# Optimization experiments

Measured on AMD Instinct MI355X. Metric: run time of the kernel, lower is better.

## Reference

```python
import jax, jax.numpy as jnp
import numpy as np

B = 8
D_MODEL = 512
N_HEADS = 8
D_HEAD = 64
D_FF = 2048
N_ENC = 4
N_DEC = 4
SRC_LEN = 512
TGT_LEN = 512
PRED_LEN = 96
SRC_SIZE = 16
TGT_SIZE = 8
EPS = 1e-5
W_SCALE = 0.02


def setup_inputs() -> dict:
    key = jax.random.key(0)
    ks = iter(jax.random.split(key, 64))

    def w(shape):
        return jax.random.normal(next(ks), shape, dtype=jnp.float32) * W_SCALE

    d, f = D_MODEL, D_FF
    inp = {
        "src": jax.random.normal(next(ks), (B, SRC_LEN, SRC_SIZE), dtype=jnp.float32),
        "tgt": jax.random.normal(next(ks), (B, TGT_LEN, TGT_SIZE), dtype=jnp.float32),
        "src_pos_emb": w((SRC_LEN, d)),
        "tgt_pos_emb": w((TGT_LEN, d)),
        "src_lin_w": w((SRC_SIZE, d)), "src_lin_b": jnp.zeros((d,), jnp.float32),
        "tgt_lin_w": w((TGT_SIZE, d)), "tgt_lin_b": jnp.zeros((d,), jnp.float32),
        # encoder stacks [N_ENC, ...]
        "enc_wq": w((N_ENC, d, d)), "enc_wk": w((N_ENC, d, d)),
        "enc_wv": w((N_ENC, d, d)), "enc_wo": w((N_ENC, d, d)),
        "enc_ff1_w": w((N_ENC, d, f)), "enc_ff1_b": jnp.zeros((N_ENC, f), jnp.float32),
        "enc_ff2_w": w((N_ENC, f, d)), "enc_ff2_b": jnp.zeros((N_ENC, d), jnp.float32),
        "enc_ln1_g": jnp.ones((N_ENC, d), jnp.float32), "enc_ln1_b": jnp.zeros((N_ENC, d), jnp.float32),
        "enc_ln2_g": jnp.ones((N_ENC, d), jnp.float32), "enc_ln2_b": jnp.zeros((N_ENC, d), jnp.float32),
        # decoder stacks [N_DEC, ...]
        "dec_sa_wq": w((N_DEC, d, d)), "dec_sa_wk": w((N_DEC, d, d)),
        "dec_sa_wv": w((N_DEC, d, d)), "dec_sa_wo": w((N_DEC, d, d)),
        "dec_ca_wq": w((N_DEC, d, d)), "dec_ca_wk": w((N_DEC, d, d)),
        "dec_ca_wv": w((N_DEC, d, d)), "dec_ca_wo": w((N_DEC, d, d)),
        "dec_ff1_w": w((N_DEC, d, f)), "dec_ff1_b": jnp.zeros((N_DEC, f), jnp.float32),
        "dec_ff2_w": w((N_DEC, f, d)), "dec_ff2_b": jnp.zeros((N_DEC, d), jnp.float32),
        "dec_ln1_g": jnp.ones((N_DEC, d), jnp.float32), "dec_ln1_b": jnp.zeros((N_DEC, d), jnp.float32),
        "dec_ln2_g": jnp.ones((N_DEC, d), jnp.float32), "dec_ln2_b": jnp.zeros((N_DEC, d), jnp.float32),
        "dec_ln3_g": jnp.ones((N_DEC, d), jnp.float32), "dec_ln3_b": jnp.zeros((N_DEC, d), jnp.float32),
        "proj_w": w((d, TGT_SIZE)), "proj_b": jnp.zeros((TGT_SIZE,), jnp.float32),
    }
    return inp


def layer_norm(x, g, b):
    mu = jnp.mean(x, axis=-1, keepdims=True)
    var = jnp.mean(jnp.square(x - mu), axis=-1, keepdims=True)
    return (x - mu) * jax.lax.rsqrt(var + EPS) * g + b


def mha(x_q, x_kv, wq, wk, wv, wo, mask):
    Bq, Lq, _ = x_q.shape
    Lk = x_kv.shape[1]
    q = (x_q @ wq).reshape(Bq, Lq, N_HEADS, D_HEAD)
    k = (x_kv @ wk).reshape(Bq, Lk, N_HEADS, D_HEAD)
    v = (x_kv @ wv).reshape(Bq, Lk, N_HEADS, D_HEAD)
    scores = jnp.einsum("bqhd,bkhd->bhqk", q, k) / jnp.sqrt(
        jnp.asarray(D_HEAD, jnp.float32))
    if mask is not None:
        scores = scores + mask  # broadcast over batch/heads
    attn = jax.nn.softmax(scores, axis=-1)
    ctx = jnp.einsum("bhqk,bkhd->bqhd", attn, v).reshape(Bq, Lq, N_HEADS * D_HEAD)
    return ctx @ wo


def dec_self_mask():
    # get_subsequence_mask with pt=0: -inf on last PRED_LEN key columns
    m = jnp.zeros((TGT_LEN, TGT_LEN), jnp.float32)
    return m.at[:, -PRED_LEN:].set(-jnp.inf)


def reference(src, tgt, src_pos_emb, tgt_pos_emb, src_lin_w, src_lin_b,
              tgt_lin_w, tgt_lin_b,
              enc_wq, enc_wk, enc_wv, enc_wo, enc_ff1_w, enc_ff1_b,
              enc_ff2_w, enc_ff2_b, enc_ln1_g, enc_ln1_b, enc_ln2_g, enc_ln2_b,
              dec_sa_wq, dec_sa_wk, dec_sa_wv, dec_sa_wo,
              dec_ca_wq, dec_ca_wk, dec_ca_wv, dec_ca_wo,
              dec_ff1_w, dec_ff1_b, dec_ff2_w, dec_ff2_b,
              dec_ln1_g, dec_ln1_b, dec_ln2_g, dec_ln2_b, dec_ln3_g, dec_ln3_b,
              proj_w, proj_b):
    # input projections + positional embedding (dropout disabled, eval mode)
    enc_x = src_pos_emb[None] + src @ src_lin_w + src_lin_b
    dec_x = tgt_pos_emb[None] + tgt @ tgt_lin_w + tgt_lin_b

    # encoder (enc_self_attn_mask is None)
    for i in range(N_ENC):
        a = mha(enc_x, enc_x, enc_wq[i], enc_wk[i], enc_wv[i], enc_wo[i], None)
        enc_x = layer_norm(a + enc_x, enc_ln1_g[i], enc_ln1_b[i])
        h = jax.nn.relu(enc_x @ enc_ff1_w[i] + enc_ff1_b[i]) @ enc_ff2_w[i] + enc_ff2_b[i]
        enc_x = layer_norm(h + enc_x, enc_ln2_g[i], enc_ln2_b[i])

    sa_mask = dec_self_mask()  # [tgt_len, tgt_len]
    for i in range(N_DEC):
        a = mha(dec_x, dec_x, dec_sa_wq[i], dec_sa_wk[i], dec_sa_wv[i],
                dec_sa_wo[i], sa_mask)
        dec_x = layer_norm(a + dec_x, dec_ln1_g[i], dec_ln1_b[i])
        a = mha(dec_x, enc_x, dec_ca_wq[i], dec_ca_wk[i], dec_ca_wv[i],
                dec_ca_wo[i], None)
        dec_x = layer_norm(a + dec_x, dec_ln2_g[i], dec_ln2_b[i])
        h = jax.nn.relu(dec_x @ dec_ff1_w[i] + dec_ff1_b[i]) @ dec_ff2_w[i] + dec_ff2_b[i]
        dec_x = layer_norm(h + dec_x, dec_ln3_g[i], dec_ln3_b[i])

    return dec_x @ proj_w + proj_b  # [B, tgt_len, tgt_size]
```

## Files before the change

### kernel.cpp

```cpp
#include <hip/hip_runtime.h>
#include <hip/hip_bf16.h>
#include <math.h>

#define D_MODEL 512
#define N_HEADS 8
#define D_HEAD  64
#define D_FF    2048
#define SEQ     512
#define BATCH   8
#define ROWS    (BATCH * SEQ)
#define PRED_LEN 96
#define KLEN_MASKED (SEQ - PRED_LEN)
#define LN_EPS  1e-5f

typedef float  f32x4 __attribute__((ext_vector_type(4)));
typedef short  s16x8 __attribute__((ext_vector_type(8)));

__device__ __forceinline__ float bf2f(ushort u) {
    union { unsigned int i; float f; } c; c.i = ((unsigned int)u) << 16; return c.f;
}
__device__ __forceinline__ ushort f2bf(float v) {
    __hip_bfloat16 h = __float2bfloat16(v);
    return *(ushort*)&h;
}
__device__ __forceinline__ void gl_lds16(const void* g, void* lds) {
    __builtin_amdgcn_global_load_lds(
        (const __attribute__((address_space(1))) unsigned int*)g,
        (__attribute__((address_space(3))) unsigned int*)lds, 16, 0, 0);
}

struct GDesc {
    const ushort* A; int lda;
    const ushort* Bt; int ldb;
    ushort* C; int ldc;
    int N; int K;
    const float* bias; int relu;
    ushort* VT; int vcol0;
};

__device__ __forceinline__ void gemm_body(const GDesc& d)
{
    __shared__ __attribute__((aligned(16))) ushort As[2][128 * 64];
    __shared__ __attribute__((aligned(16))) ushort Bs[2][64 * 64];
    const int tid = threadIdx.x;
    const int w = tid >> 6, lane = tid & 63;
    const int l16 = lane & 15, quad = lane >> 4;
    const int m0 = blockIdx.y * 128, n0 = blockIdx.x * 64;
    const ushort* Ab = d.A + (size_t)m0 * d.lda;
    const ushort* Bb = d.Bt + (size_t)n0 * d.ldb;
    const int wm = (w >> 1) * 64, wn = (w & 1) * 32;
    const int nk = d.K >> 6;
    const int lr = lane >> 3, lc = lane & 7;
    const int ch = lc ^ lr;

    auto stage = [&](int buf, int k0) {
        #pragma unroll
        for (int q = 0; q < 4; ++q) {
            int seg = q * 4 + w;
            int row = seg * 8 + lr;
            gl_lds16(Ab + (size_t)row * d.lda + k0 + ch * 8,
                     (void*)(As[buf] + seg * 512));
        }
        #pragma unroll
        for (int q = 0; q < 2; ++q) {
            int seg = q * 4 + w;
            int row = seg * 8 + lr;
            gl_lds16(Bb + (size_t)row * d.ldb + k0 + ch * 8,
                     (void*)(Bs[buf] + seg * 512));
        }
    };

    f32x4 acc[4][2];
    #pragma unroll
    for (int i = 0; i < 4; ++i)
        #pragma unroll
        for (int j = 0; j < 2; ++j) acc[i][j] = (f32x4)0.f;

    auto compute = [&](int buf) {
        #pragma unroll
        for (int t2 = 0; t2 < 2; ++t2) {
            s16x8 af[4];
            #pragma unroll
            for (int i = 0; i < 4; ++i) {
                int r = wm + i * 16 + l16;
                int p = (t2 * 4 + quad) ^ (r & 7);
                af[i] = *(const s16x8*)(As[buf] + r * 64 + p * 8);
            }
            #pragma unroll
            for (int j = 0; j < 2; ++j) {
                int r = wn + j * 16 + l16;
                int p = (t2 * 4 + quad) ^ (r & 7);
                s16x8 bfr = *(const s16x8*)(Bs[buf] + r * 64 + p * 8);
                #pragma unroll
                for (int i = 0; i < 4; ++i)
                    acc[i][j] = __builtin_amdgcn_mfma_f32_16x16x32_bf16(af[i], bfr, acc[i][j], 0, 0, 0);
            }
        }
    };

    stage(0, 0);
    __syncthreads();
    int cur = 0;
    for (int t = 0; t < nk - 1; ++t) {
        stage(cur ^ 1, (t + 1) << 6);
        compute(cur);
        __syncthreads();
        cur ^= 1;
    }
    compute(cur);

    const bool isv = (d.VT != nullptr) && (n0 >= d.vcol0);
    if (isv) {
        #pragma unroll
        for (int i = 0; i < 4; ++i) {
            int mrow = m0 + wm + i * 16 + quad * 4;
            int b = mrow >> 9, pbase = mrow & 511;
            #pragma unroll
            for (int j = 0; j < 2; ++j) {
                int cv = n0 + wn + j * 16 + l16 - d.vcol0;
                int h = cv >> 6, dd = cv & 63;
                union { ushort u[4]; uint2 v; } pk;
                #pragma unroll
                for (int r = 0; r < 4; ++r) pk.u[r] = f2bf(acc[i][j][r]);
                *(uint2*)(d.VT + ((size_t)((b * 8 + h) * 64 + dd) * 512 + pbase)) = pk.v;
            }
        }
    } else {
        #pragma unroll
        for (int i = 0; i < 4; ++i) {
            #pragma unroll
            for (int j = 0; j < 2; ++j) {
                int col = n0 + wn + j * 16 + l16;
                float bv = d.bias ? d.bias[col] : 0.f;
                #pragma unroll
                for (int r = 0; r < 4; ++r) {
                    float v = acc[i][j][r] + bv;
                    if (d.relu) v = fmaxf(v, 0.f);
                    d.C[(size_t)(m0 + wm + i * 16 + quad * 4 + r) * d.ldc + col] = f2bf(v);
                }
            }
        }
    }
}

__global__ __launch_bounds__(256) void gemm_one(GDesc d)
{
    if ((int)(blockIdx.x * 64) < d.N) gemm_body(d);
}

__global__ __launch_bounds__(256) void gemm_two(GDesc d0, GDesc d1)
{
    const GDesc& d = blockIdx.z ? d1 : d0;
    if ((int)(blockIdx.x * 64) < d.N) gemm_body(d);
}

struct SKDesc {
    const ushort* A; int lda;
    const ushort* Bt; int ldb;
    float* P;
    int K;
};

__global__ __launch_bounds__(256) void gemm_sk(SKDesc d)
{
    __shared__ __attribute__((aligned(16))) ushort As[2][128 * 64];
    __shared__ __attribute__((aligned(16))) ushort Bs[2][64 * 64];
    const int tid = threadIdx.x;
    const int w = tid >> 6, lane = tid & 63;
    const int l16 = lane & 15, quad = lane >> 4;
    const int m0 = blockIdx.y * 128, n0 = blockIdx.x * 64;
    const int slice = blockIdx.z;
    const int kb = slice * (d.K >> 1);
    const int nk = d.K >> 7;
    const ushort* Ab = d.A + (size_t)m0 * d.lda + kb;
    const ushort* Bb = d.Bt + (size_t)n0 * d.ldb + kb;
    const int wm = (w >> 1) * 64, wn = (w & 1) * 32;
    const int lr = lane >> 3, lc = lane & 7;
    const int ch = lc ^ lr;

    auto stage = [&](int buf, int k0) {
        #pragma unroll
        for (int q = 0; q < 4; ++q) {
            int seg = q * 4 + w;
            int row = seg * 8 + lr;
            gl_lds16(Ab + (size_t)row * d.lda + k0 + ch * 8,
                     (void*)(As[buf] + seg * 512));
        }
        #pragma unroll
        for (int q = 0; q < 2; ++q) {
            int seg = q * 4 + w;
            int row = seg * 8 + lr;
            gl_lds16(Bb + (size_t)row * d.ldb + k0 + ch * 8,
                     (void*)(Bs[buf] + seg * 512));
        }
    };

    f32x4 acc[4][2];
    #pragma unroll
    for (int i = 0; i < 4; ++i)
        #pragma unroll
        for (int j = 0; j < 2; ++j) acc[i][j] = (f32x4)0.f;

    auto compute = [&](int buf) {
        #pragma unroll
        for (int t2 = 0; t2 < 2; ++t2) {
            s16x8 af[4];
            #pragma unroll
            for (int i = 0; i < 4; ++i) {
                int r = wm + i * 16 + l16;
                int p = (t2 * 4 + quad) ^ (r & 7);
                af[i] = *(const s16x8*)(As[buf] + r * 64 + p * 8);
            }
            #pragma unroll
            for (int j = 0; j < 2; ++j) {
                int r = wn + j * 16 + l16;
                int p = (t2 * 4 + quad) ^ (r & 7);
                s16x8 bfr = *(const s16x8*)(Bs[buf] + r * 64 + p * 8);
                #pragma unroll
                for (int i = 0; i < 4; ++i)
                    acc[i][j] = __builtin_amdgcn_mfma_f32_16x16x32_bf16(af[i], bfr, acc[i][j], 0, 0, 0);
            }
        }
    };

    stage(0, 0);
    __syncthreads();
    int cur = 0;
    for (int t = 0; t < nk - 1; ++t) {
        stage(cur ^ 1, (t + 1) << 6);
        compute(cur);
        __syncthreads();
        cur ^= 1;
    }
    compute(cur);

    float* P = d.P + (size_t)slice * ((size_t)ROWS * 512);
    #pragma unroll
    for (int i = 0; i < 4; ++i) {
        #pragma unroll
        for (int j = 0; j < 2; ++j) {
            int col = n0 + wn + j * 16 + l16;
            #pragma unroll
            for (int r = 0; r < 4; ++r)
                P[(size_t)(m0 + wm + i * 16 + quad * 4 + r) * 512 + col] = acc[i][j][r];
        }
    }
}

__global__ __launch_bounds__(256) void flash_attn(
    const ushort* __restrict__ Q, int ldq,
    const ushort* __restrict__ K, int ldk,
    const ushort* __restrict__ Vt,
    ushort* __restrict__ O, int ldo, int klen)
{
    __shared__ __attribute__((aligned(16))) ushort KVs[8192];
    __shared__ __attribute__((aligned(16))) ushort Es[4][2048];
    const int tid = threadIdx.x, w = tid >> 6, lane = tid & 63;
    const int l16 = lane & 15, quad = lane >> 4;
    const int bh = blockIdx.y, b = bh >> 3, h = bh & 7;
    const int q0 = blockIdx.x * 64;

    const ushort* Qb = Q + (size_t)(b * SEQ) * ldq + h * D_HEAD;
    const ushort* Kb = K + (size_t)(b * SEQ) * ldk + h * D_HEAD;

    s16x8 af0, af1;
    {
        const ushort* qr = Qb + (size_t)(q0 + w * 16 + l16) * ldq + quad * 8;
        af0 = *(const s16x8*)(qr);
        af1 = *(const s16x8*)(qr + 32);
    }

    f32x4 sc[32];

    #pragma unroll
    for (int kc = 0; kc < 4; ++kc) {
        #pragma unroll
        for (int it = 0; it < 4; ++it) {
            int cc = (it * 4 + w) * 64 + lane;
            int row = cc >> 3;
            int dch = (cc & 7) ^ (row & 7);
            gl_lds16(Kb + (size_t)(kc * 128 + row) * ldk + dch * 8,
                     (void*)(KVs + (size_t)(it * 4 + w) * 512));
        }
        __syncthreads();
        #pragma unroll
        for (int kt = 0; kt < 8; ++kt) {
            int r0 = kt * 16 + l16;
            s16x8 b0 = *(const s16x8*)(KVs + r0 * 64 + ((quad)     ^ (r0 & 7)) * 8);
            s16x8 b1 = *(const s16x8*)(KVs + r0 * 64 + ((4 + quad) ^ (r0 & 7)) * 8);
            f32x4 a = __builtin_amdgcn_mfma_f32_16x16x32_bf16(af0, b0, (f32x4)0.f, 0, 0, 0);
            sc[kc * 8 + kt] = __builtin_amdgcn_mfma_f32_16x16x32_bf16(af1, b1, a, 0, 0, 0);
        }
        __syncthreads();
    }

    float inv[4];
    #pragma unroll
    for (int r = 0; r < 4; ++r) {
        float m = -1e30f;
        #pragma unroll
        for (int j = 0; j < 32; ++j) {
            bool valid = (j * 16 + l16) < klen;
            m = valid ? fmaxf(m, sc[j][r]) : m;
        }
        m = fmaxf(m, __shfl_xor(m, 1));
        m = fmaxf(m, __shfl_xor(m, 2));
        m = fmaxf(m, __shfl_xor(m, 4));
        m = fmaxf(m, __shfl_xor(m, 8));
        float ssum = 0.f;
        #pragma unroll
        for (int j = 0; j < 32; ++j) {
            bool valid = (j * 16 + l16) < klen;
            float e = valid ? __expf((sc[j][r] - m) * 0.125f) : 0.f;
            sc[j][r] = e;
            ssum += e;
        }
        ssum += __shfl_xor(ssum, 1);
        ssum += __shfl_xor(ssum, 2);
        ssum += __shfl_xor(ssum, 4);
        ssum += __shfl_xor(ssum, 8);
        inv[r] = 1.f / ssum;
    }

    f32x4 oacc[4];
    #pragma unroll
    for (int jd = 0; jd < 4; ++jd) oacc[jd] = (f32x4)0.f;
    const ushort* Vb = Vt + (size_t)bh * (D_HEAD * SEQ);
    #pragma unroll
    for (int kc = 0; kc < 4; ++kc) {
        #pragma unroll
        for (int it = 0; it < 4; ++it) {
            int cc = (it * 4 + w) * 64 + lane;
            int d = cc >> 4;
            int kch = (cc & 15) ^ (d & 15);
            gl_lds16(Vb + (size_t)d * SEQ + kc * 128 + kch * 8,
                     (void*)(KVs + (size_t)(it * 4 + w) * 512));
        }
        #pragma unroll
        for (int j = 0; j < 8; ++j) {
            int lcj = j * 2 + (l16 >> 3);
            #pragma unroll
            for (int r = 0; r < 4; ++r) {
                int m = quad * 4 + r;
                Es[w][m * 128 + (lcj ^ m) * 8 + (l16 & 7)] = f2bf(sc[kc * 8 + j][r]);
            }
        }
        __syncthreads();
        #pragma unroll
        for (int ks = 0; ks < 4; ++ks) {
            int lc = ks * 4 + quad;
            s16x8 ea = *(const s16x8*)(&Es[w][l16 * 128 + (lc ^ l16) * 8]);
            #pragma unroll
            for (int jd = 0; jd < 4; ++jd) {
                int row = jd * 16 + l16;
                s16x8 vb = *(const s16x8*)(KVs + row * 128 + (lc ^ l16) * 8);
                oacc[jd] = __builtin_amdgcn_mfma_f32_16x16x32_bf16(ea, vb, oacc[jd], 0, 0, 0);
            }
        }
        __syncthreads();
    }

    ushort* Ob = O + (size_t)(b * SEQ) * ldo + h * D_HEAD;
    #pragma unroll
    for (int jd = 0; jd < 4; ++jd)
        #pragma unroll
        for (int r = 0; r < 4; ++r)
            Ob[(size_t)(q0 + w * 16 + quad * 4 + r) * ldo + jd * 16 + l16] =
                f2bf(oacc[jd][r] * inv[r]);
}

struct AttnPtrs { const float* p[48]; };
struct FfPtrs   { const float* p[16]; };

__global__ __launch_bounds__(256) void repack_attn(AttnPtrs L, ushort* __restrict__ out)
{
    int z = blockIdx.z;
    const float* in = L.p[z];
    ushort* o = out + (size_t)z * 262144;
    __shared__ float t[32][33];
    int n0 = blockIdx.x * 32, k0 = blockIdx.y * 32;
    int tx = threadIdx.x & 31, ty = threadIdx.x >> 5;
    #pragma unroll
    for (int r = 0; r < 4; ++r)
        t[ty + r * 8][tx] = in[(size_t)(k0 + ty + r * 8) * 512 + n0 + tx];
    __syncthreads();
    #pragma unroll
    for (int r = 0; r < 4; ++r)
        o[(size_t)(n0 + ty + r * 8) * 512 + k0 + tx] = f2bf(t[tx][ty + r * 8]);
}

__global__ __launch_bounds__(256) void repack_ff(FfPtrs L, ushort* __restrict__ out)
{
    int z = blockIdx.y;
    int Kd = (z < 8) ? 512 : 2048, Nd = (z < 8) ? 2048 : 512;
    const float* in = L.p[z];
    ushort* o = out + (size_t)z * (512 * 2048);
    int t = blockIdx.x;
    int tn = Nd / 32;
    int n0 = (t % tn) * 32, k0 = (t / tn) * 32;
    __shared__ float ts[32][33];
    int tx = threadIdx.x & 31, ty = threadIdx.x >> 5;
    #pragma unroll
    for (int r = 0; r < 4; ++r)
        ts[ty + r * 8][tx] = in[(size_t)(k0 + ty + r * 8) * Nd + n0 + tx];
    __syncthreads();
    #pragma unroll
    for (int r = 0; r < 4; ++r)
        o[(size_t)(n0 + ty + r * 8) * Kd + k0 + tx] = f2bf(ts[tx][ty + r * 8]);
}

__global__ __launch_bounds__(256) void input_proj2(
    const float* __restrict__ x0, const float* __restrict__ w0,
    const float* __restrict__ b0, const float* __restrict__ p0,
    float* __restrict__ o0_32, ushort* __restrict__ o0_b, int in0,
    const float* __restrict__ x1, const float* __restrict__ w1,
    const float* __restrict__ b1, const float* __restrict__ p1,
    float* __restrict__ o1_32, ushort* __restrict__ o1_b, int in1)
{
    const int z = blockIdx.y;
    const float* x = z ? x1 : x0;  const float* w = z ? w1 : w0;
    const float* bias = z ? b1 : b0; const float* pos = z ? p1 : p0;
    float* out32 = z ? o1_32 : o0_32; ushort* outb = z ? o1_b : o0_b;
    int in_size = z ? in1 : in0;
    int idx = blockIdx.x * 256 + threadIdx.x;
    int col = idx & (D_MODEL - 1);
    int row = idx >> 9;
    int l   = row & (SEQ - 1);
    const float* xr = x + (size_t)row * in_size;
    float acc = bias[col] + pos[(size_t)l * D_MODEL + col];
    for (int t = 0; t < in_size; ++t) acc += xr[t] * w[(size_t)t * D_MODEL + col];
    out32[idx] = acc;
    outb[idx]  = f2bf(acc);
}

__global__ __launch_bounds__(256) void add_ln2(
    const float* __restrict__ p, const float* __restrict__ gb,
    const float* __restrict__ x,
    const float* __restrict__ g, const float* __restrict__ b,
    float* __restrict__ out32, ushort* __restrict__ outb)
{
    const int row  = blockIdx.x * 4 + (threadIdx.x >> 6);
    const int lane = threadIdx.x & 63;
    const int c0   = lane * 8;
    const size_t base = (size_t)row * D_MODEL + c0;
    const float* p1 = p + (size_t)ROWS * 512;
    f32x4 a0 = *(const f32x4*)(p + base),  a1 = *(const f32x4*)(p + base + 4);
    f32x4 c0v= *(const f32x4*)(p1 + base), c1v= *(const f32x4*)(p1 + base + 4);
    f32x4 x0 = *(const f32x4*)(x + base),  x1 = *(const f32x4*)(x + base + 4);
    float v[8];
    #pragma unroll
    for (int j = 0; j < 4; ++j) {
        v[j]     = a0[j] + c0v[j] + x0[j];
        v[4 + j] = a1[j] + c1v[j] + x1[j];
    }
    if (gb) {
        f32x4 gb0 = *(const f32x4*)(gb + c0), gb1 = *(const f32x4*)(gb + c0 + 4);
        #pragma unroll
        for (int j = 0; j < 4; ++j) { v[j] += gb0[j]; v[4 + j] += gb1[j]; }
    }
    float s = 0.f;
    #pragma unroll
    for (int j = 0; j < 8; ++j) s += v[j];
    #pragma unroll
    for (int off = 32; off; off >>= 1) s += __shfl_xor(s, off);
    float mu = s * (1.f / D_MODEL);
    float q = 0.f;
    #pragma unroll
    for (int j = 0; j < 8; ++j) { v[j] -= mu; q += v[j] * v[j]; }
    #pragma unroll
    for (int off = 32; off; off >>= 1) q += __shfl_xor(q, off);
    float rs = rsqrtf(q * (1.f / D_MODEL) + LN_EPS);
    f32x4 g0 = *(const f32x4*)(g + c0), g1 = *(const f32x4*)(g + c0 + 4);
    f32x4 b0 = *(const f32x4*)(b + c0), b1 = *(const f32x4*)(b + c0 + 4);
    f32x4 y0, y1;
    union { ushort u[8]; s16x8 w; } pk;
    #pragma unroll
    for (int j = 0; j < 4; ++j) {
        y0[j] = v[j]     * rs * g0[j] + b0[j];
        y1[j] = v[4 + j] * rs * g1[j] + b1[j];
        pk.u[j]     = f2bf(y0[j]);
        pk.u[4 + j] = f2bf(y1[j]);
    }
    *(f32x4*)(out32 + base)     = y0;
    *(f32x4*)(out32 + base + 4) = y1;
    *(s16x8*)(outb + base)      = pk.w;
}

__global__ __launch_bounds__(256) void final_proj(
    const float* __restrict__ X, const float* __restrict__ W,
    const float* __restrict__ b, float* __restrict__ out)
{
    const int row  = blockIdx.x * 4 + (threadIdx.x >> 6);
    const int lane = threadIdx.x & 63;
    const float* xr = X + (size_t)row * D_MODEL + lane * 8;
    f32x4 x0 = *(const f32x4*)(xr), x1 = *(const f32x4*)(xr + 4);
    const float* wr = W + (size_t)lane * 64;
    f32x4 pa = (f32x4)0.f, pb = (f32x4)0.f;
    #pragma unroll
    for (int j = 0; j < 8; ++j) {
        float xv = (j < 4) ? x0[j] : x1[j - 4];
        f32x4 w0 = *(const f32x4*)(wr + j * 8);
        f32x4 w1 = *(const f32x4*)(wr + j * 8 + 4);
        #pragma unroll
        for (int c = 0; c < 4; ++c) { pa[c] += xv * w0[c]; pb[c] += xv * w1[c]; }
    }
    #pragma unroll
    for (int off = 32; off; off >>= 1) {
        #pragma unroll
        for (int c = 0; c < 4; ++c) {
            pa[c] += __shfl_xor(pa[c], off);
            pb[c] += __shfl_xor(pb[c], off);
        }
    }
    if (lane == 0) {
        float* o = out + (size_t)row * 8;
        #pragma unroll
        for (int c = 0; c < 4; ++c) { o[c] = pa[c] + b[c]; o[4 + c] = pb[c] + b[4 + c]; }
    }
}

extern "C" void kernel_launch(void* const* d_in, const int* in_sizes, int n_in,
                              void* d_out, int out_size, void* d_ws, size_t ws_size,
                              hipStream_t stream)
{
    const float* src         = (const float*)d_in[0];
    const float* tgt         = (const float*)d_in[1];
    const float* src_pos     = (const float*)d_in[2];
    const float* tgt_pos     = (const float*)d_in[3];
    const float* src_lin_w   = (const float*)d_in[4];
    const float* src_lin_b   = (const float*)d_in[5];
    const float* tgt_lin_w   = (const float*)d_in[6];
    const float* tgt_lin_b   = (const float*)d_in[7];
    const float* enc_wq      = (const float*)d_in[8];
    const float* enc_wk      = (const float*)d_in[9];
    const float* enc_wv      = (const float*)d_in[10];
    const float* enc_wo      = (const float*)d_in[11];
    const float* enc_ff1_w   = (const float*)d_in[12];
    const float* enc_ff1_b   = (const float*)d_in[13];
    const float* enc_ff2_w   = (const float*)d_in[14];
    const float* enc_ff2_b   = (const float*)d_in[15];
    const float* enc_ln1_g   = (const float*)d_in[16];
    const float* enc_ln1_b   = (const float*)d_in[17];
    const float* enc_ln2_g   = (const float*)d_in[18];
    const float* enc_ln2_b   = (const float*)d_in[19];
    const float* dec_sa_wq   = (const float*)d_in[20];
    const float* dec_sa_wk   = (const float*)d_in[21];
    const float* dec_sa_wv   = (const float*)d_in[22];
    const float* dec_sa_wo   = (const float*)d_in[23];
    const float* dec_ca_wq   = (const float*)d_in[24];
    const float* dec_ca_wk   = (const float*)d_in[25];
    const float* dec_ca_wv   = (const float*)d_in[26];
    const float* dec_ca_wo   = (const float*)d_in[27];
    const float* dec_ff1_w   = (const float*)d_in[28];
    const float* dec_ff1_b   = (const float*)d_in[29];
    const float* dec_ff2_w   = (const float*)d_in[30];
    const float* dec_ff2_b   = (const float*)d_in[31];
    const float* dec_ln1_g   = (const float*)d_in[32];
    const float* dec_ln1_b   = (const float*)d_in[33];
    const float* dec_ln2_g   = (const float*)d_in[34];
    const float* dec_ln2_b   = (const float*)d_in[35];
    const float* dec_ln3_g   = (const float*)d_in[36];
    const float* dec_ln3_b   = (const float*)d_in[37];
    const float* proj_w      = (const float*)d_in[38];
    const float* proj_b      = (const float*)d_in[39];

    char* p = (char*)d_ws;
    auto carve = [&](size_t bytes) { char* r = p; p += (bytes + 255) & ~(size_t)255; return r; };
    ushort* enc_xb = (ushort*)carve((size_t)ROWS * D_MODEL * 2);
    ushort* dec_xb = (ushort*)carve((size_t)ROWS * D_MODEL * 2);
    float*  enc_x32= (float*) carve((size_t)ROWS * D_MODEL * 4);
    float*  dec_x32= (float*) carve((size_t)ROWS * D_MODEL * 4);
    ushort* qkvb   = (ushort*)carve((size_t)ROWS * 1536 * 2);
    ushort* qb     = (ushort*)carve((size_t)ROWS * D_MODEL * 2);
    ushort* kvb    = (ushort*)carve((size_t)ROWS * 1024 * 2);
    ushort* ctxb   = (ushort*)carve((size_t)ROWS * D_MODEL * 2);
    float*  pf     = (float*) carve((size_t)2 * ROWS * D_MODEL * 4);
    ushort* ffhb   = (ushort*)carve((size_t)ROWS * D_FF * 2);
    ushort* vt     = (ushort*)carve((size_t)64 * D_HEAD * SEQ * 2);
    ushort* wa     = (ushort*)carve((size_t)48 * 262144 * 2);
    ushort* wf     = (ushort*)carve((size_t)16 * 1048576 * 2);

    const dim3 blk(256);

    {
        AttnPtrs A;
        for (int i = 0; i < 4; ++i) {
            const size_t o = (size_t)i * 262144;
            A.p[i * 3 + 0] = enc_wq + o;  A.p[i * 3 + 1] = enc_wk + o;  A.p[i * 3 + 2] = enc_wv + o;
            A.p[12 + i] = enc_wo + o;
            A.p[16 + i * 3 + 0] = dec_sa_wq + o; A.p[16 + i * 3 + 1] = dec_sa_wk + o;
            A.p[16 + i * 3 + 2] = dec_sa_wv + o;
            A.p[28 + i] = dec_sa_wo + o;
            A.p[32 + i * 2 + 0] = dec_ca_wk + o; A.p[32 + i * 2 + 1] = dec_ca_wv + o;
            A.p[40 + i] = dec_ca_wq + o;
            A.p[44 + i] = dec_ca_wo + o;
        }
        repack_attn<<<dim3(16, 16, 48), blk, 0, stream>>>(A, wa);
        FfPtrs F;
        for (int i = 0; i < 4; ++i) {
            F.p[0 + i]  = enc_ff1_w + (size_t)i * 1048576;
            F.p[4 + i]  = dec_ff1_w + (size_t)i * 1048576;
            F.p[8 + i]  = enc_ff2_w + (size_t)i * 1048576;
            F.p[12 + i] = dec_ff2_w + (size_t)i * 1048576;
        }
        repack_ff<<<dim3(1024, 16), blk, 0, stream>>>(F, wf);
    }

    auto mkd = [&](const ushort* A, int lda, const ushort* Bt, int ldb,
                   ushort* C, int ldc, int N, int K,
                   const float* bias, int relu, ushort* VT, int vcol0) {
        GDesc d; d.A = A; d.lda = lda; d.Bt = Bt; d.ldb = ldb;
        d.C = C; d.ldc = ldc; d.N = N; d.K = K;
        d.bias = bias; d.relu = relu; d.VT = VT; d.vcol0 = vcol0;
        return d;
    };
    auto g64 = [&](const GDesc& d) {
        gemm_one<<<dim3(d.N / 64, ROWS / 128), blk, 0, stream>>>(d);
    };
    auto gsk = [&](const ushort* A, int lda, const ushort* Bt, int K) {
        SKDesc d; d.A = A; d.lda = lda; d.Bt = Bt; d.ldb = K; d.P = pf; d.K = K;
        gemm_sk<<<dim3(8, ROWS / 128, 2), blk, 0, stream>>>(d);
    };

    input_proj2<<<dim3(ROWS * D_MODEL / 256, 2), blk, 0, stream>>>(
        src, src_lin_w, src_lin_b, src_pos, enc_x32, enc_xb, 16,
        tgt, tgt_lin_w, tgt_lin_b, tgt_pos, dec_x32, dec_xb, 8);

    for (int i = 0; i < 4; ++i) {
        g64(mkd(enc_xb, 512, wa + (size_t)(i * 3) * 262144, 512, qkvb, 1536,
                1536, 512, nullptr, 0, vt, 1024));
        flash_attn<<<dim3(8, 64), blk, 0, stream>>>(qkvb, 1536, qkvb + 512, 1536, vt,
                                                    ctxb, D_MODEL, SEQ);
        gsk(ctxb, 512, wa + (size_t)(12 + i) * 262144, 512);
        add_ln2<<<ROWS / 4, blk, 0, stream>>>(pf, nullptr, enc_x32,
                                              enc_ln1_g + i * 512, enc_ln1_b + i * 512,
                                              enc_x32, enc_xb);
        g64(mkd(enc_xb, 512, wf + (size_t)i * 1048576, 512, ffhb, 2048,
                2048, 512, enc_ff1_b + i * 2048, 1, nullptr, 0));
        gsk(ffhb, 2048, wf + (size_t)(8 + i) * 1048576, 2048);
        add_ln2<<<ROWS / 4, blk, 0, stream>>>(pf, enc_ff2_b + i * 512, enc_x32,
                                              enc_ln2_g + i * 512, enc_ln2_b + i * 512,
                                              enc_x32, enc_xb);
    }

    for (int i = 0; i < 4; ++i) {
        g64(mkd(dec_xb, 512, wa + (size_t)(16 + i * 3) * 262144, 512, qkvb, 1536,
                1536, 512, nullptr, 0, vt, 1024));
        flash_attn<<<dim3(8, 64), blk, 0, stream>>>(qkvb, 1536, qkvb + 512, 1536, vt,
                                                    ctxb, D_MODEL, KLEN_MASKED);
        gsk(ctxb, 512, wa + (size_t)(28 + i) * 262144, 512);
        add_ln2<<<ROWS / 4, blk, 0, stream>>>(pf, nullptr, dec_x32,
                                              dec_ln1_g + i * 512, dec_ln1_b + i * 512,
                                              dec_x32, dec_xb);
        {
            GDesc dq = mkd(dec_xb, 512, wa + (size_t)(40 + i) * 262144, 512, qb, 512,
                           512, 512, nullptr, 0, nullptr, 0);
            GDesc dkv = mkd(enc_xb, 512, wa + (size_t)(32 + i * 2) * 262144, 512, kvb, 1024,
                            1024, 512, nullptr, 0, vt, 512);
            gemm_two<<<dim3(16, ROWS / 128, 2), blk, 0, stream>>>(dq, dkv);
        }
        flash_attn<<<dim3(8, 64), blk, 0, stream>>>(qb, 512, kvb, 1024, vt,
                                                    ctxb, D_MODEL, SEQ);
        gsk(ctxb, 512, wa + (size_t)(44 + i) * 262144, 512);
        add_ln2<<<ROWS / 4, blk, 0, stream>>>(pf, nullptr, dec_x32,
                                              dec_ln2_g + i * 512, dec_ln2_b + i * 512,
                                              dec_x32, dec_xb);
        g64(mkd(dec_xb, 512, wf + (size_t)(4 + i) * 1048576, 512, ffhb, 2048,
                2048, 512, dec_ff1_b + i * 2048, 1, nullptr, 0));
        gsk(ffhb, 2048, wf + (size_t)(12 + i) * 1048576, 2048);
        add_ln2<<<ROWS / 4, blk, 0, stream>>>(pf, dec_ff2_b + i * 512, dec_x32,
                                              dec_ln3_g + i * 512, dec_ln3_b + i * 512,
                                              dec_x32, dec_xb);
    }

    final_proj<<<ROWS / 4, blk, 0, stream>>>(dec_x32, proj_w, proj_b, (float*)d_out);
}
```

Before: 1.354 ms.

## Double-buffer K/V tiles in flash attention and split-K GEMM four ways

The flash attention kernel now double-buffers K and V tiles in shared memory, prefetching the next 128-key chunk while the current one runs through MFMA, which drops one barrier per chunk. The split-K GEMM used for output and FF2 projections moves from 2 to 4 K slices, doubling grid parallelism, and add_ln2 now sums four partial buffers. This should hide global load latency and raise occupancy, at the cost of twice the LDS for KV tiles and extra partial-sum traffic through a workspace twice as large.

After: 1.486 ms. 9.8% more time.

```diff
diff --git a/kernel.cpp b/kernel.cpp
--- a/kernel.cpp
+++ b/kernel.cpp
@@ -170,8 +170,8 @@
     const int l16 = lane & 15, quad = lane >> 4;
     const int m0 = blockIdx.y * 128, n0 = blockIdx.x * 64;
     const int slice = blockIdx.z;
-    const int kb = slice * (d.K >> 1);
-    const int nk = d.K >> 7;
+    const int kb = slice * (d.K >> 2);
+    const int nk = d.K >> 8;
     const ushort* Ab = d.A + (size_t)m0 * d.lda + kb;
     const ushort* Bb = d.Bt + (size_t)n0 * d.ldb + kb;
     const int wm = (w >> 1) * 64, wn = (w & 1) * 32;
@@ -253,7 +253,7 @@
     const ushort* __restrict__ Vt,
     ushort* __restrict__ O, int ldo, int klen)
 {
-    __shared__ __attribute__((aligned(16))) ushort KVs[8192];
+    __shared__ __attribute__((aligned(16))) ushort KV[2][8192];
     __shared__ __attribute__((aligned(16))) ushort Es[4][2048];
     const int tid = threadIdx.x, w = tid >> 6, lane = tid & 63;
     const int l16 = lane & 15, quad = lane >> 4;
@@ -262,6 +262,30 @@
 
     const ushort* Qb = Q + (size_t)(b * SEQ) * ldq + h * D_HEAD;
     const ushort* Kb = K + (size_t)(b * SEQ) * ldk + h * D_HEAD;
+    const ushort* Vb = Vt + (size_t)bh * (D_HEAD * SEQ);
+
+    auto stageK = [&](int buf, int kc) {
+        #pragma unroll
+        for (int it = 0; it < 4; ++it) {
+            int cc = (it * 4 + w) * 64 + lane;
+            int row = cc >> 3;
+            int dch = (cc & 7) ^ (row & 7);
+            gl_lds16(Kb + (size_t)(kc * 128 + row) * ldk + dch * 8,
+                     (void*)(KV[buf] + (size_t)(it * 4 + w) * 512));
+        }
+    };
+    auto stageV = [&](int buf, int kc) {
+        #pragma unroll
+        for (int it = 0; it < 4; ++it) {
+            int cc = (it * 4 + w) * 64 + lane;
+            int dd = cc >> 4;
+            int kch = (cc & 15) ^ (dd & 15);
+            gl_lds16(Vb + (size_t)dd * SEQ + kc * 128 + kch * 8,
+                     (void*)(KV[buf] + (size_t)(it * 4 + w) * 512));
+        }
+    };
+
+    stageK(0, 0);
 
     s16x8 af0, af1;
     {
@@ -271,28 +295,24 @@
     }
 
     f32x4 sc[32];
-
+    __syncthreads();
+    int buf = 0;
     #pragma unroll
     for (int kc = 0; kc < 4; ++kc) {
-        #pragma unroll
-        for (int it = 0; it < 4; ++it) {
-            int cc = (it * 4 + w) * 64 + lane;
-            int row = cc >> 3;
-            int dch = (cc & 7) ^ (row & 7);
-            gl_lds16(Kb + (size_t)(kc * 128 + row) * ldk + dch * 8,
-                     (void*)(KVs + (size_t)(it * 4 + w) * 512));
-        }
-        __syncthreads();
+        if (kc < 3) stageK(buf ^ 1, kc + 1);
         #pragma unroll
         for (int kt = 0; kt < 8; ++kt) {
             int r0 = kt * 16 + l16;
-            s16x8 b0 = *(const s16x8*)(KVs + r0 * 64 + ((quad)     ^ (r0 & 7)) * 8);
-            s16x8 b1 = *(const s16x8*)(KVs + r0 * 64 + ((4 + quad) ^ (r0 & 7)) * 8);
+            s16x8 b0 = *(const s16x8*)(KV[buf] + r0 * 64 + ((quad)     ^ (r0 & 7)) * 8);
+            s16x8 b1 = *(const s16x8*)(KV[buf] + r0 * 64 + ((4 + quad) ^ (r0 & 7)) * 8);
             f32x4 a = __builtin_amdgcn_mfma_f32_16x16x32_bf16(af0, b0, (f32x4)0.f, 0, 0, 0);
             sc[kc * 8 + kt] = __builtin_amdgcn_mfma_f32_16x16x32_bf16(af1, b1, a, 0, 0, 0);
         }
         __syncthreads();
-    }
+        buf ^= 1;
+    }
+
+    stageV(0, 0);
 
     float inv[4];
     #pragma unroll
@@ -325,17 +345,12 @@
     f32x4 oacc[4];
     #pragma unroll
     for (int jd = 0; jd < 4; ++jd) oacc[jd] = (f32x4)0.f;
-    const ushort* Vb = Vt + (size_t)bh * (D_HEAD * SEQ);
+
+    __syncthreads();
+    buf = 0;
     #pragma unroll
     for (int kc = 0; kc < 4; ++kc) {
-        #pragma unroll
-        for (int it = 0; it < 4; ++it) {
-            int cc = (it * 4 + w) * 64 + lane;
-            int d = cc >> 4;
-            int kch = (cc & 15) ^ (d & 15);
-            gl_lds16(Vb + (size_t)d * SEQ + kc * 128 + kch * 8,
-                     (void*)(KVs + (size_t)(it * 4 + w) * 512));
-        }
+        if (kc < 3) stageV(buf ^ 1, kc + 1);
         #pragma unroll
         for (int j = 0; j < 8; ++j) {
             int lcj = j * 2 + (l16 >> 3);
@@ -345,7 +360,6 @@
                 Es[w][m * 128 + (lcj ^ m) * 8 + (l16 & 7)] = f2bf(sc[kc * 8 + j][r]);
             }
         }
-        __syncthreads();
         #pragma unroll
         for (int ks = 0; ks < 4; ++ks) {
             int lc = ks * 4 + quad;
@@ -353,11 +367,12 @@
             #pragma unroll
             for (int jd = 0; jd < 4; ++jd) {
                 int row = jd * 16 + l16;
-                s16x8 vb = *(const s16x8*)(KVs + row * 128 + (lc ^ l16) * 8);
+                s16x8 vb = *(const s16x8*)(KV[buf] + row * 128 + (lc ^ l16) * 8);
                 oacc[jd] = __builtin_amdgcn_mfma_f32_16x16x32_bf16(ea, vb, oacc[jd], 0, 0, 0);
             }
         }
         __syncthreads();
+        buf ^= 1;
     }
 
     ushort* Ob = O + (size_t)(b * SEQ) * ldo + h * D_HEAD;
@@ -443,15 +458,19 @@
     const int lane = threadIdx.x & 63;
     const int c0   = lane * 8;
     const size_t base = (size_t)row * D_MODEL + c0;
-    const float* p1 = p + (size_t)ROWS * 512;
-    f32x4 a0 = *(const f32x4*)(p + base),  a1 = *(const f32x4*)(p + base + 4);
-    f32x4 c0v= *(const f32x4*)(p1 + base), c1v= *(const f32x4*)(p1 + base + 4);
-    f32x4 x0 = *(const f32x4*)(x + base),  x1 = *(const f32x4*)(x + base + 4);
+    const size_t SL = (size_t)ROWS * 512;
     float v[8];
-    #pragma unroll
-    for (int j = 0; j < 4; ++j) {
-        v[j]     = a0[j] + c0v[j] + x0[j];
-        v[4 + j] = a1[j] + c1v[j] + x1[j];
+    {
+        f32x4 s0 = *(const f32x4*)(p + base),          s1 = *(const f32x4*)(p + base + 4);
+        f32x4 t0 = *(const f32x4*)(p + SL + base),     t1 = *(const f32x4*)(p + SL + base + 4);
+        f32x4 u0 = *(const f32x4*)(p + 2*SL + base),   u1 = *(const f32x4*)(p + 2*SL + base + 4);
+        f32x4 w0 = *(const f32x4*)(p + 3*SL + base),   w1 = *(const f32x4*)(p + 3*SL + base + 4);
+        f32x4 x0 = *(const f32x4*)(x + base),          x1 = *(const f32x4*)(x + base + 4);
+        #pragma unroll
+        for (int j = 0; j < 4; ++j) {
+            v[j]     = s0[j] + t0[j] + u0[j] + w0[j] + x0[j];
+            v[4 + j] = s1[j] + t1[j] + u1[j] + w1[j] + x1[j];
+        }
     }
     if (gb) {
         f32x4 gb0 = *(const f32x4*)(gb + c0), gb1 = *(const f32x4*)(gb + c0 + 4);
@@ -574,7 +593,7 @@
     ushort* qb     = (ushort*)carve((size_t)ROWS * D_MODEL * 2);
     ushort* kvb    = (ushort*)carve((size_t)ROWS * 1024 * 2);
     ushort* ctxb   = (ushort*)carve((size_t)ROWS * D_MODEL * 2);
-    float*  pf     = (float*) carve((size_t)2 * ROWS * D_MODEL * 4);
+    float*  pf     = (float*) carve((size_t)4 * ROWS * D_MODEL * 4);
     ushort* ffhb   = (ushort*)carve((size_t)ROWS * D_FF * 2);
     ushort* vt     = (ushort*)carve((size_t)64 * D_HEAD * SEQ * 2);
     ushort* wa     = (ushort*)carve((size_t)48 * 262144 * 2);
@@ -619,7 +638,7 @@
     };
     auto gsk = [&](const ushort* A, int lda, const ushort* Bt, int K) {
         SKDesc d; d.A = A; d.lda = lda; d.Bt = Bt; d.ldb = K; d.P = pf; d.K = K;
-        gemm_sk<<<dim3(8, ROWS / 128, 2), blk, 0, stream>>>(d);
+        gemm_sk<<<dim3(8, ROWS / 128, 4), blk, 0, stream>>>(d);
     };
 
     input_proj2<<<dim3(ROWS * D_MODEL / 256, 2), blk, 0, stream>>>(
```
